# Optimization experiments

Measured on AMD Instinct MI355X. Metric: run time of the kernel, lower is better.

## Reference

```python
import jax, jax.numpy as jnp
import numpy as np

TOP_K_FRACTION = 0.1


def setup_inputs() -> dict:
    key = jax.random.key(0)
    k1, k2, k3 = jax.random.split(key, 3)
    B, H, S, D = 2, 12, 1024, 64
    q = jax.random.normal(k1, (B, H, S, D), dtype=jnp.float32)
    k = jax.random.normal(k2, (B, H, S, D), dtype=jnp.float32)
    v = jax.random.normal(k3, (B, H, S, D), dtype=jnp.float32)
    mask = jnp.zeros((B, 1, 1, S), dtype=jnp.float32)
    return {"q": q, "k": k, "v": v, "mask": mask}


def reference(q, k, v, mask):
    B, H, S, D = q.shape
    k_precise = max(1, int(S * TOP_K_FRACTION))
    # binary (sign) approximation of attention scores; detached like torch
    q_bin = jnp.sign(jax.lax.stop_gradient(q))
    k_bin = jnp.sign(jax.lax.stop_gradient(k))
    approx_scores = jnp.einsum('bhsd,bhtd->bhst', q_bin, k_bin) / D  # [B,H,S,S]
    _, topk_idx = jax.lax.top_k(approx_scores, k_precise)  # [B,H,S,kp]
    # gather top-k keys/values per query: [B,H,S,kp,D]
    k_gathered = jnp.take_along_axis(k[:, :, None, :, :], topk_idx[..., None], axis=3)
    v_gathered = jnp.take_along_axis(v[:, :, None, :, :], topk_idx[..., None], axis=3)
    scale = np.float32(1.0 / np.sqrt(D))
    precise_scores = jnp.einsum('bhsd,bhskd->bhsk', q, k_gathered) * scale
    # gather mask along key positions: mask [B,1,1,S] -> [B,H,S,kp]
    mask_gathered = jnp.take_along_axis(
        jnp.broadcast_to(mask, (B, H, S, S)), topk_idx, axis=-1)
    precise_scores = precise_scores + mask_gathered
    precise_probs = jax.nn.softmax(precise_scores, axis=-1)
    attn_output = jnp.einsum('bhsk,bhskd->bhsd', precise_probs, v_gathered)
    return attn_output
```

## Files before the change

kernel.cpp:

```cpp
#include <hip/hip_runtime.h>
#include <hip/hip_fp16.h>
#include <cstdint>

#define BB 2
#define HH 12
#define SS 1024
#define DD 64
#define KP 102
#define CHK 64
#define KROW 72
#define COMBW 65

typedef _Float16 half8v  __attribute__((ext_vector_type(8)));
typedef float    float4v __attribute__((ext_vector_type(4)));
typedef unsigned long long u64;

__device__ __forceinline__ int mbcnt64(u64 m) {
    return (int)__builtin_amdgcn_mbcnt_hi((unsigned)(m >> 32),
               __builtin_amdgcn_mbcnt_lo((unsigned)(m & 0xffffffffull), 0u));
}
template <int CTRL>
__device__ __forceinline__ float dpp_f(float x) {
    return __builtin_bit_cast(float,
        __builtin_amdgcn_update_dpp(0, __builtin_bit_cast(int, x), CTRL, 0xF, 0xF, false));
}
__device__ __forceinline__ float row16_sum(float x) {
    x += dpp_f<0xB1>(x);
    x += dpp_f<0x4E>(x);
    x += dpp_f<0x141>(x);
    x += dpp_f<0x140>(x);
    return x;
}

__global__ __launch_bounds__(256) void pack_kernel(
    const float* __restrict__ k, const float* __restrict__ v,
    u64* __restrict__ kbits, _Float16* __restrict__ kh, _Float16* __restrict__ vT)
{
    __shared__ __align__(16) _Float16 vt_lds[DD * KROW];
    const int tid  = (int)threadIdx.x;
    const int w    = tid >> 6;
    const int lane = tid & 63;
    const int bh = (int)blockIdx.x >> 4;
    const int t0 = ((int)blockIdx.x & 15) * 64;

    const float* kbase = k + ((size_t)bh * SS + t0) * DD;
    const float* vbase = v + ((size_t)bh * SS + t0) * DD;
    #pragma unroll 1
    for (int i = 0; i < 16; ++i) {
        int rl = w * 16 + i;
        float kv = kbase[rl * DD + lane];
        float vv = vbase[rl * DD + lane];
        u64 km = __ballot(kv > 0.0f);
        kh[((size_t)bh * SS + t0 + rl) * DD + lane] = (_Float16)kv;
        vt_lds[lane * KROW + rl] = (_Float16)vv;
        if (lane == 0) kbits[(size_t)bh * SS + t0 + rl] = km;
    }
    __syncthreads();
    #pragma unroll
    for (int it = 0; it < 2; ++it) {
        int s = tid + it * 256;
        int d = s >> 3, c8 = s & 7;
        *(half8v*)(vT + ((size_t)bh * DD + d) * SS + t0 + c8 * 8) =
            *(const half8v*)(&vt_lds[d * KROW + c8 * 8]);
    }
}

__global__ __launch_bounds__(512, 4) void battn_kernel(
    const float* __restrict__ q, const _Float16* __restrict__ kh,
    const _Float16* __restrict__ vT, const float* __restrict__ mask,
    const u64* __restrict__ kbits, float* __restrict__ out)
{
    const int tid  = (int)threadIdx.x;
    const int w    = tid >> 6;
    const int lane = tid & 63;
    const int bh    = (int)blockIdx.x >> 4;
    const int qtile = (int)blockIdx.x & 15;
    const int bidx  = bh / HH;
    const int qr    = lane & 15;
    const int quad  = lane >> 4;
    const int half  = w >> 2;
    const int wq    = w & 3;

    __shared__ __align__(16) char smem[65536];
    _Float16* K0  = (_Float16*)(smem);
    _Float16* VT0 = (_Float16*)(smem + 9216);
    _Float16* K1  = (_Float16*)(smem + 18432);
    _Float16* VT1 = (_Float16*)(smem + 27648);
    _Float16* Pw  = (_Float16*)(smem + 36864) + w * 16 * KROW;
    u64*      sel = (u64*)(smem + 55296);
    _Float16* mlds = (_Float16*)(smem + 63488);
    float* combA = (float*)(smem);
    float* combL = (float*)(smem + 64 * COMBW * 4);

    {
        float2 mv = *(const float2*)(mask + (size_t)bidx * SS + tid * 2);
        mlds[tid * 2]     = (_Float16)(mv.x - 4.0f);
        mlds[tid * 2 + 1] = (_Float16)(mv.y - 4.0f);
    }

    const float* qblock = q + ((size_t)bh * SS + qtile * 64) * DD;
    {
        const u64* kb = kbits + (size_t)bh * SS;
        u64 kbreg[16];
        #pragma unroll
        for (int j = 0; j < 16; ++j) kbreg[j] = kb[j * 64 + lane];
        #pragma unroll 1
        for (int qq = 0; qq < 8; ++qq) {
            const int ql = w * 8 + qq;
            float qv = qblock[ql * DD + lane];
            u64 qm = __ballot(qv > 0.0f);
            int pbin[16];
            #pragma unroll
            for (int j = 0; j < 16; ++j) pbin[j] = (int)__popcll(qm ^ kbreg[j]);
            #define COUNT_LE(P, OUTC)                                      \
                { int _c = 0;                                              \
                  _Pragma("unroll")                                        \
                  for (int j = 0; j < 16; ++j)                             \
                      _c += (int)__popcll(__ballot(pbin[j] <= (P)));       \
                  (OUTC) = _c; }
            int P = 27, c, clt;
            COUNT_LE(P, c);
            if (c >= KP) {
                COUNT_LE(P - 1, clt);
                while (clt >= KP) { c = clt; --P; COUNT_LE(P - 1, clt); }
            } else {
                do { clt = c; ++P; COUNT_LE(P, c); } while (c < KP);
            }
            const int binP = P;
            const int need = KP - clt;
            #undef COUNT_LE
            u64 my_tm = 0; int tie_base = 0;
            #pragma unroll
            for (int j = 0; j < 16; ++j) {
                bool isGt  = pbin[j] < binP;
                bool isTie = (pbin[j] == binP);
                u64 tiem = __ballot(isTie);
                int rank = tie_base + mbcnt64(tiem);
                bool take = isGt || (isTie && rank < need);
                u64 tm = __ballot(take);
                if (lane == j) my_tm = tm;
                tie_base += (int)__popcll(tiem);
            }
            if (lane < 16) sel[ql * 16 + lane] = my_tm;
        }
    }

    half8v qa0, qa1;
    {
        const float* qf = qblock + (wq * 16 + qr) * DD + quad * 8;
        #pragma unroll
        for (int j = 0; j < 8; ++j) {
            qa0[j] = (_Float16)(qf[j] * 0.125f);
            qa1[j] = (_Float16)(qf[32 + j] * 0.125f);
        }
    }

    const _Float16* khead  = kh + (size_t)bh * SS * DD;
    const _Float16* vthead = vT + (size_t)bh * DD * SS;
    const int srow = tid >> 3, sc8 = tid & 7;

    float4v acc[4];
    #pragma unroll
    for (int dt = 0; dt < 4; ++dt) { acc[dt][0]=0.f; acc[dt][1]=0.f; acc[dt][2]=0.f; acc[dt][3]=0.f; }
    float lp[4] = {0.f, 0.f, 0.f, 0.f};

    #pragma unroll 1
    for (int it = 0; it < 8; ++it) {
        __syncthreads();
        *(half8v*)(K0  + srow * KROW + sc8 * 8) =
            *(const half8v*)(khead + (size_t)(it * CHK + srow) * DD + sc8 * 8);
        *(half8v*)(K1  + srow * KROW + sc8 * 8) =
            *(const half8v*)(khead + (size_t)((it + 8) * CHK + srow) * DD + sc8 * 8);
        *(half8v*)(VT0 + srow * KROW + sc8 * 8) =
            *(const half8v*)(vthead + (size_t)srow * SS + it * CHK + sc8 * 8);
        *(half8v*)(VT1 + srow * KROW + sc8 * 8) =
            *(const half8v*)(vthead + (size_t)srow * SS + (it + 8) * CHK + sc8 * 8);
        __syncthreads();

        const _Float16* KL = half ? K1 : K0;
        const _Float16* VL = half ? VT1 : VT0;
        const int ch = half * 8 + it;

        #pragma unroll
        for (int nt = 0; nt < 4; ++nt) {
            const _Float16* klp = KL + (nt * 16 + qr) * KROW + quad * 8;
            half8v b0 = *(const half8v*)klp;
            half8v b1 = *(const half8v*)(klp + 32);
            float4v cfr; cfr[0]=0.f; cfr[1]=0.f; cfr[2]=0.f; cfr[3]=0.f;
            cfr = __builtin_amdgcn_mfma_f32_16x16x32_f16(qa0, b0, cfr, 0, 0, 0);
            cfr = __builtin_amdgcn_mfma_f32_16x16x32_f16(qa1, b1, cfr, 0, 0, 0);
            const int tg = ch * CHK + nt * 16 + qr;
            const float mk = (float)mlds[tg];
            #pragma unroll
            for (int r = 0; r < 4; ++r) {
                const int qlr = wq * 16 + quad * 4 + r;
                unsigned sm = ((const unsigned*)sel)[qlr * 32 + (tg >> 5)];
                float e = ((sm >> (tg & 31)) & 1u) ? __expf(cfr[r] + mk) : 0.0f;
                lp[r] += e;
                Pw[(quad * 4 + r) * KROW + nt * 16 + qr] = (_Float16)e;
            }
        }

        half8v pa0 = *(const half8v*)(Pw + qr * KROW + quad * 8);
        half8v pa1 = *(const half8v*)(Pw + qr * KROW + 32 + quad * 8);
        #pragma unroll
        for (int dt = 0; dt < 4; ++dt) {
            const _Float16* vl = VL + (dt * 16 + qr) * KROW + quad * 8;
            acc[dt] = __builtin_amdgcn_mfma_f32_16x16x32_f16(pa0, *(const half8v*)vl,        acc[dt], 0, 0, 0);
            acc[dt] = __builtin_amdgcn_mfma_f32_16x16x32_f16(pa1, *(const half8v*)(vl + 32), acc[dt], 0, 0, 0);
        }
    }

    __syncthreads();
    #pragma unroll
    for (int r = 0; r < 4; ++r) lp[r] = row16_sum(lp[r]);
    if (half == 0) {
        if (qr == 0) {
            #pragma unroll
            for (int r = 0; r < 4; ++r) combL[wq * 16 + quad * 4 + r] = lp[r];
        }
        #pragma unroll
        for (int dt = 0; dt < 4; ++dt)
            #pragma unroll
            for (int r = 0; r < 4; ++r)
                combA[(wq * 16 + quad * 4 + r) * COMBW + dt * 16 + qr] = acc[dt][r];
    }
    __syncthreads();
    if (half == 1) {
        float rinv[4];
        #pragma unroll
        for (int r = 0; r < 4; ++r)
            rinv[r] = __frcp_rn(lp[r] + combL[wq * 16 + quad * 4 + r]);
        float* orow = out + ((size_t)bh * SS + qtile * 64 + wq * 16) * DD;
        #pragma unroll
        for (int dt = 0; dt < 4; ++dt)
            #pragma unroll
            for (int r = 0; r < 4; ++r)
                orow[(quad * 4 + r) * DD + dt * 16 + qr] =
                    (acc[dt][r] + combA[(wq * 16 + quad * 4 + r) * COMBW + dt * 16 + qr]) * rinv[r];
    }
}

extern "C" void kernel_launch(void* const* d_in, const int* in_sizes, int n_in,
                              void* d_out, int out_size, void* d_ws, size_t ws_size,
                              hipStream_t stream) {
    const float* q    = (const float*)d_in[0];
    const float* k    = (const float*)d_in[1];
    const float* v    = (const float*)d_in[2];
    const float* mask = (const float*)d_in[3];
    float* out = (float*)d_out;

    const int rows = BB * HH * SS;
    u64* kbits = (u64*)d_ws;
    _Float16* kh = (_Float16*)((char*)d_ws + (size_t)rows * sizeof(u64));
    _Float16* vT = kh + (size_t)rows * DD;

    pack_kernel<<<rows / 64, 256, 0, stream>>>(k, v, kbits, kh, vT);
    battn_kernel<<<BB * HH * (SS / 64), 512, 0, stream>>>(q, kh, vT, mask, kbits, out);
}
```

Measured before the change: 117.0 us.

## Split top-k selection into separate kernel and register-prefetch K/V chunks

Moves the binary-score top-k selection out of the attention kernel into a dedicated select_kernel that writes a per-query bitmask to workspace. Each selection block now handles 16 queries, so the launch has many more blocks. The attention kernel drops from 512 to 256 threads: each wave processes all 16 chunks for its 16 queries, which removes the two-half split and the LDS combine step at the end. Global K/V loads are now prefetched into registers one chunk ahead, and the mask is read directly from global memory. The cost is an extra kernel launch, a bitmask round trip through global memory, and half the threads per attention block.

```diff
diff --git a/kernel.cpp b/kernel.cpp
--- a/kernel.cpp
+++ b/kernel.cpp
@@ -9,7 +9,7 @@
 #define KP 102
 #define CHK 64
 #define KROW 72
-#define COMBW 65
+#define SELW 17
 
 typedef _Float16 half8v  __attribute__((ext_vector_type(8)));
 typedef float    float4v __attribute__((ext_vector_type(4)));
@@ -65,10 +65,66 @@
     }
 }
 
-__global__ __launch_bounds__(512, 4) void battn_kernel(
+__global__ __launch_bounds__(256) void select_kernel(
+    const float* __restrict__ q, const u64* __restrict__ kbits,
+    u64* __restrict__ selbm)
+{
+    const int tid  = (int)threadIdx.x;
+    const int w    = tid >> 6;
+    const int lane = tid & 63;
+    const int qbase = (int)blockIdx.x * 16 + w * 4;
+    const int bh    = qbase >> 10;
+
+    const u64* kb = kbits + (size_t)bh * SS;
+    u64 kbreg[16];
+    #pragma unroll
+    for (int j = 0; j < 16; ++j) kbreg[j] = kb[j * 64 + lane];
+
+    #pragma unroll 1
+    for (int qq = 0; qq < 4; ++qq) {
+        const int qid = qbase + qq;
+        float qv = q[(size_t)qid * DD + lane];
+        u64 qm = __ballot(qv > 0.0f);
+        int pbin[16];
+        #pragma unroll
+        for (int j = 0; j < 16; ++j) pbin[j] = (int)__popcll(qm ^ kbreg[j]);
+        #define COUNT_LE(P, OUTC)                                      \
+            { int _c = 0;                                              \
+              _Pragma("unroll")                                        \
+              for (int j = 0; j < 16; ++j)                             \
+                  _c += (int)__popcll(__ballot(pbin[j] <= (P)));       \
+              (OUTC) = _c; }
+        int P = 27, c, clt;
+        COUNT_LE(P, c);
+        if (c >= KP) {
+            COUNT_LE(P - 1, clt);
+            while (clt >= KP) { c = clt; --P; COUNT_LE(P - 1, clt); }
+        } else {
+            do { clt = c; ++P; COUNT_LE(P, c); } while (c < KP);
+        }
+        const int binP = P;
+        const int need = KP - clt;
+        #undef COUNT_LE
+        u64 my_tm = 0; int tie_base = 0;
+        #pragma unroll
+        for (int j = 0; j < 16; ++j) {
+            bool isGt  = pbin[j] < binP;
+            bool isTie = (pbin[j] == binP);
+            u64 tiem = __ballot(isTie);
+            int rank = tie_base + mbcnt64(tiem);
+            bool take = isGt || (isTie && rank < need);
+            u64 tm = __ballot(take);
+            if (lane == j) my_tm = tm;
+            tie_base += (int)__popcll(tiem);
+        }
+        if (lane < 16) selbm[(size_t)qid * 16 + lane] = my_tm;
+    }
+}
+
+__global__ __launch_bounds__(256, 2) void battn_kernel(
     const float* __restrict__ q, const _Float16* __restrict__ kh,
     const _Float16* __restrict__ vT, const float* __restrict__ mask,
-    const u64* __restrict__ kbits, float* __restrict__ out)
+    const u64* __restrict__ selbm, float* __restrict__ out)
 {
     const int tid  = (int)threadIdx.x;
     const int w    = tid >> 6;
@@ -78,76 +134,23 @@
     const int bidx  = bh / HH;
     const int qr    = lane & 15;
     const int quad  = lane >> 4;
-    const int half  = w >> 2;
-    const int wq    = w & 3;
-
-    __shared__ __align__(16) char smem[65536];
-    _Float16* K0  = (_Float16*)(smem);
-    _Float16* VT0 = (_Float16*)(smem + 9216);
-    _Float16* K1  = (_Float16*)(smem + 18432);
-    _Float16* VT1 = (_Float16*)(smem + 27648);
-    _Float16* Pw  = (_Float16*)(smem + 36864) + w * 16 * KROW;
-    u64*      sel = (u64*)(smem + 55296);
-    _Float16* mlds = (_Float16*)(smem + 63488);
-    float* combA = (float*)(smem);
-    float* combL = (float*)(smem + 64 * COMBW * 4);
-
-    {
-        float2 mv = *(const float2*)(mask + (size_t)bidx * SS + tid * 2);
-        mlds[tid * 2]     = (_Float16)(mv.x - 4.0f);
-        mlds[tid * 2 + 1] = (_Float16)(mv.y - 4.0f);
+
+    __shared__ __align__(16) _Float16 K_lds[CHK * KROW];
+    __shared__ __align__(16) _Float16 VT_lds[DD * KROW];
+    __shared__ __align__(16) _Float16 P_lds[4][16 * KROW];
+    __shared__ u64 sel[64 * SELW];
+
+    #pragma unroll
+    for (int it = 0; it < 4; ++it) {
+        int s = tid + it * 256;
+        int ql = s >> 4, j = s & 15;
+        sel[ql * SELW + j] = selbm[((size_t)bh * SS + qtile * 64 + ql) * 16 + j];
     }
 
     const float* qblock = q + ((size_t)bh * SS + qtile * 64) * DD;
-    {
-        const u64* kb = kbits + (size_t)bh * SS;
-        u64 kbreg[16];
-        #pragma unroll
-        for (int j = 0; j < 16; ++j) kbreg[j] = kb[j * 64 + lane];
-        #pragma unroll 1
-        for (int qq = 0; qq < 8; ++qq) {
-            const int ql = w * 8 + qq;
-            float qv = qblock[ql * DD + lane];
-            u64 qm = __ballot(qv > 0.0f);
-            int pbin[16];
-            #pragma unroll
-            for (int j = 0; j < 16; ++j) pbin[j] = (int)__popcll(qm ^ kbreg[j]);
-            #define COUNT_LE(P, OUTC)                                      \
-                { int _c = 0;                                              \
-                  _Pragma("unroll")                                        \
-                  for (int j = 0; j < 16; ++j)                             \
-                      _c += (int)__popcll(__ballot(pbin[j] <= (P)));       \
-                  (OUTC) = _c; }
-            int P = 27, c, clt;
-            COUNT_LE(P, c);
-            if (c >= KP) {
-                COUNT_LE(P - 1, clt);
-                while (clt >= KP) { c = clt; --P; COUNT_LE(P - 1, clt); }
-            } else {
-                do { clt = c; ++P; COUNT_LE(P, c); } while (c < KP);
-            }
-            const int binP = P;
-            const int need = KP - clt;
-            #undef COUNT_LE
-            u64 my_tm = 0; int tie_base = 0;
-            #pragma unroll
-            for (int j = 0; j < 16; ++j) {
-                bool isGt  = pbin[j] < binP;
-                bool isTie = (pbin[j] == binP);
-                u64 tiem = __ballot(isTie);
-                int rank = tie_base + mbcnt64(tiem);
-                bool take = isGt || (isTie && rank < need);
-                u64 tm = __ballot(take);
-                if (lane == j) my_tm = tm;
-                tie_base += (int)__popcll(tiem);
-            }
-            if (lane < 16) sel[ql * 16 + lane] = my_tm;
-        }
-    }
-
     half8v qa0, qa1;
     {
-        const float* qf = qblock + (wq * 16 + qr) * DD + quad * 8;
+        const float* qf = qblock + (w * 16 + qr) * DD + quad * 8;
         #pragma unroll
         for (int j = 0; j < 8; ++j) {
             qa0[j] = (_Float16)(qf[j] * 0.125f);
@@ -157,7 +160,16 @@
 
     const _Float16* khead  = kh + (size_t)bh * SS * DD;
     const _Float16* vthead = vT + (size_t)bh * DD * SS;
-    const int srow = tid >> 3, sc8 = tid & 7;
+    const float*    mrow   = mask + (size_t)bidx * SS;
+    const int s0 = tid, s1 = tid + 256;
+    const int r0 = s0 >> 3, c0 = (s0 & 7) * 8;
+    const int r1 = s1 >> 3, c1 = (s1 & 7) * 8;
+
+    half8v kp0, kp1, vp0, vp1;
+    kp0 = *(const half8v*)(khead + (size_t)(0 * CHK + r0) * DD + c0);
+    kp1 = *(const half8v*)(khead + (size_t)(0 * CHK + r1) * DD + c1);
+    vp0 = *(const half8v*)(vthead + (size_t)r0 * SS + 0 * CHK + c0);
+    vp1 = *(const half8v*)(vthead + (size_t)r1 * SS + 0 * CHK + c1);
 
     float4v acc[4];
     #pragma unroll
@@ -165,80 +177,62 @@
     float lp[4] = {0.f, 0.f, 0.f, 0.f};
 
     #pragma unroll 1
-    for (int it = 0; it < 8; ++it) {
+    for (int ch = 0; ch < 16; ++ch) {
         __syncthreads();
-        *(half8v*)(K0  + srow * KROW + sc8 * 8) =
-            *(const half8v*)(khead + (size_t)(it * CHK + srow) * DD + sc8 * 8);
-        *(half8v*)(K1  + srow * KROW + sc8 * 8) =
-            *(const half8v*)(khead + (size_t)((it + 8) * CHK + srow) * DD + sc8 * 8);
-        *(half8v*)(VT0 + srow * KROW + sc8 * 8) =
-            *(const half8v*)(vthead + (size_t)srow * SS + it * CHK + sc8 * 8);
-        *(half8v*)(VT1 + srow * KROW + sc8 * 8) =
-            *(const half8v*)(vthead + (size_t)srow * SS + (it + 8) * CHK + sc8 * 8);
+        *(half8v*)(&K_lds[r0 * KROW + c0])  = kp0;
+        *(half8v*)(&K_lds[r1 * KROW + c1])  = kp1;
+        *(half8v*)(&VT_lds[r0 * KROW + c0]) = vp0;
+        *(half8v*)(&VT_lds[r1 * KROW + c1]) = vp1;
         __syncthreads();
 
-        const _Float16* KL = half ? K1 : K0;
-        const _Float16* VL = half ? VT1 : VT0;
-        const int ch = half * 8 + it;
+        if (ch < 15) {
+            kp0 = *(const half8v*)(khead + (size_t)((ch + 1) * CHK + r0) * DD + c0);
+            kp1 = *(const half8v*)(khead + (size_t)((ch + 1) * CHK + r1) * DD + c1);
+            vp0 = *(const half8v*)(vthead + (size_t)r0 * SS + (ch + 1) * CHK + c0);
+            vp1 = *(const half8v*)(vthead + (size_t)r1 * SS + (ch + 1) * CHK + c1);
+        }
 
         #pragma unroll
         for (int nt = 0; nt < 4; ++nt) {
-            const _Float16* klp = KL + (nt * 16 + qr) * KROW + quad * 8;
+            const _Float16* klp = &K_lds[(nt * 16 + qr) * KROW + quad * 8];
             half8v b0 = *(const half8v*)klp;
             half8v b1 = *(const half8v*)(klp + 32);
             float4v cfr; cfr[0]=0.f; cfr[1]=0.f; cfr[2]=0.f; cfr[3]=0.f;
             cfr = __builtin_amdgcn_mfma_f32_16x16x32_f16(qa0, b0, cfr, 0, 0, 0);
             cfr = __builtin_amdgcn_mfma_f32_16x16x32_f16(qa1, b1, cfr, 0, 0, 0);
             const int tg = ch * CHK + nt * 16 + qr;
-            const float mk = (float)mlds[tg];
+            const float mk = mrow[tg] - 4.0f;
+            const int u32i = (tg >> 5) & 1;
+            const int wj   = tg >> 6;
             #pragma unroll
             for (int r = 0; r < 4; ++r) {
-                const int qlr = wq * 16 + quad * 4 + r;
-                unsigned sm = ((const unsigned*)sel)[qlr * 32 + (tg >> 5)];
+                const int ql = w * 16 + quad * 4 + r;
+                unsigned sm = ((const unsigned*)&sel[ql * SELW + wj])[u32i];
                 float e = ((sm >> (tg & 31)) & 1u) ? __expf(cfr[r] + mk) : 0.0f;
                 lp[r] += e;
-                Pw[(quad * 4 + r) * KROW + nt * 16 + qr] = (_Float16)e;
+                P_lds[w][(quad * 4 + r) * KROW + nt * 16 + qr] = (_Float16)e;
             }
         }
 
-        half8v pa0 = *(const half8v*)(Pw + qr * KROW + quad * 8);
-        half8v pa1 = *(const half8v*)(Pw + qr * KROW + 32 + quad * 8);
+        half8v pa0 = *(const half8v*)(&P_lds[w][qr * KROW + quad * 8]);
+        half8v pa1 = *(const half8v*)(&P_lds[w][qr * KROW + 32 + quad * 8]);
         #pragma unroll
         for (int dt = 0; dt < 4; ++dt) {
-            const _Float16* vl = VL + (dt * 16 + qr) * KROW + quad * 8;
+            const _Float16* vl = &VT_lds[(dt * 16 + qr) * KROW + quad * 8];
             acc[dt] = __builtin_amdgcn_mfma_f32_16x16x32_f16(pa0, *(const half8v*)vl,        acc[dt], 0, 0, 0);
             acc[dt] = __builtin_amdgcn_mfma_f32_16x16x32_f16(pa1, *(const half8v*)(vl + 32), acc[dt], 0, 0, 0);
         }
     }
 
-    __syncthreads();
-    #pragma unroll
-    for (int r = 0; r < 4; ++r) lp[r] = row16_sum(lp[r]);
-    if (half == 0) {
-        if (qr == 0) {
-            #pragma unroll
-            for (int r = 0; r < 4; ++r) combL[wq * 16 + quad * 4 + r] = lp[r];
-        }
-        #pragma unroll
-        for (int dt = 0; dt < 4; ++dt)
-            #pragma unroll
-            for (int r = 0; r < 4; ++r)
-                combA[(wq * 16 + quad * 4 + r) * COMBW + dt * 16 + qr] = acc[dt][r];
-    }
-    __syncthreads();
-    if (half == 1) {
-        float rinv[4];
+    float rinv[4];
+    #pragma unroll
+    for (int r = 0; r < 4; ++r) rinv[r] = __frcp_rn(row16_sum(lp[r]));
+    float* orow = out + ((size_t)bh * SS + qtile * 64 + w * 16) * DD;
+    #pragma unroll
+    for (int dt = 0; dt < 4; ++dt)
         #pragma unroll
         for (int r = 0; r < 4; ++r)
-            rinv[r] = __frcp_rn(lp[r] + combL[wq * 16 + quad * 4 + r]);
-        float* orow = out + ((size_t)bh * SS + qtile * 64 + wq * 16) * DD;
-        #pragma unroll
-        for (int dt = 0; dt < 4; ++dt)
-            #pragma unroll
-            for (int r = 0; r < 4; ++r)
-                orow[(quad * 4 + r) * DD + dt * 16 + qr] =
-                    (acc[dt][r] + combA[(wq * 16 + quad * 4 + r) * COMBW + dt * 16 + qr]) * rinv[r];
-    }
+            orow[(quad * 4 + r) * DD + dt * 16 + qr] = acc[dt][r] * rinv[r];
 }
 
 extern "C" void kernel_launch(void* const* d_in, const int* in_sizes, int n_in,
@@ -254,7 +248,9 @@
     u64* kbits = (u64*)d_ws;
     _Float16* kh = (_Float16*)((char*)d_ws + (size_t)rows * sizeof(u64));
     _Float16* vT = kh + (size_t)rows * DD;
+    u64* selbm = (u64*)(vT + (size_t)rows * DD);
 
     pack_kernel<<<rows / 64, 256, 0, stream>>>(k, v, kbits, kh, vT);
-    battn_kernel<<<BB * HH * (SS / 64), 512, 0, stream>>>(q, kh, vT, mask, kbits, out);
-}
+    select_kernel<<<rows / 16, 256, 0, stream>>>(q, kbits, selbm);
+    battn_kernel<<<BB * HH * (SS / 64), 256, 0, stream>>>(q, kh, vT, mask, selbm, out);
+}
```

Result: no change. 118.2 us (+1.1%).
